# Performance work log

Hardware: AMD Instinct MI355X
Metric: run time of the kernel (lower is better)

## Reference

```python
import jax, jax.numpy as jnp
import numpy as np

N_STEPS = 2
MAX_STEP = 1.0
EPS64 = float(np.finfo(np.float64).eps)


def _sphere_log(p, q):
    # log map on unit sphere, tangent at p pointing to q; p,q: [..., D]
    cos = jnp.clip(jnp.sum(p * q, axis=-1, keepdims=True), -1.0, 1.0)
    u = q - cos * p
    un = jnp.linalg.norm(u, axis=-1, keepdims=True)
    theta = jnp.arccos(cos)
    return theta * u / (un + 1e-12)


def _sphere_exp(p, v):
    # exp map on unit sphere; jnp.sinc(n/pi) = sin(n)/n (stable at 0)
    n = jnp.linalg.norm(v, axis=-1, keepdims=True)
    x = jnp.cos(n) * p + jnp.sinc(n / jnp.pi) * v
    return x / jnp.linalg.norm(x, axis=-1, keepdims=True)


def setup_inputs() -> dict:
    key = jax.random.key(0)
    ks = jax.random.split(key, 6)
    N, C, D, E = 50000, 16, 3, 1600000
    nodes = jax.random.normal(ks[0], (N, C, D), dtype=jnp.float32)
    nodes = nodes / jnp.linalg.norm(nodes, axis=-1, keepdims=True)  # points on S^2
    edge_w = jax.random.uniform(ks[1], (E,), dtype=jnp.float32)
    senders = jax.random.randint(ks[2], (E,), 0, N, dtype=jnp.int32)
    receivers = jax.random.randint(ks[3], (E,), 0, N, dtype=jnp.int32)
    t_sqrt = 1.0 + 0.3 * jax.random.normal(ks[4], (C,), dtype=jnp.float32)
    delta_sqrt = 1.0 + 0.3 * jax.random.normal(ks[5], (C,), dtype=jnp.float32)
    return {"nodes": nodes, "edge_w": edge_w, "t_sqrt": t_sqrt,
            "delta_sqrt": delta_sqrt, "senders": senders, "receivers": receivers}


def reference(nodes, edge_w, t_sqrt, delta_sqrt, senders, receivers):
    N = nodes.shape[0]
    t = (t_sqrt ** 2) / N_STEPS            # per-channel time, split across Euler steps
    delta = delta_sqrt ** 2                 # per-channel min step size
    deg = jax.ops.segment_sum(edge_w, senders, num_segments=N)  # [N]

    def laplace(x):
        # graph Laplacian of manifold-valued signal: weighted mean of log maps, negated
        logs = _sphere_log(x[senders], x[receivers])              # [E, C, D]
        agg = jax.ops.segment_sum(edge_w[:, None, None] * logs, senders, num_segments=N)
        return -agg / (deg[:, None, None] + 1e-12)                # [N, C, D]

    def step(x, _):
        v = laplace(x)
        nrm = jnp.sqrt(jnp.sum(v * v, axis=-1) + EPS64)           # [N, C]
        alp = jax.nn.sigmoid(nrm - delta[None, :])
        scale = jnp.where(nrm * alp <= MAX_STEP, alp, MAX_STEP / nrm)
        v = -(v * scale[..., None]) * t[None, :, None]
        return _sphere_exp(x, v), None

    x, _ = jax.lax.scan(step, nodes, None, length=N_STEPS, unroll=N_STEPS)
    return x
```

## Files before the change

kernel.cpp:

```cpp
#include <hip/hip_runtime.h>
#include <math.h>


constexpr float EPS64F = 2.2204460492503131e-16f;
constexpr float PI_F   = 3.14159265358979323846f;
constexpr int   NREP   = 8;

typedef int   vi4 __attribute__((ext_vector_type(4)));
typedef float vf4 __attribute__((ext_vector_type(4)));

__global__ __launch_bounds__(256) void hist_kernel(
    const vi4* __restrict__ snd4, int* __restrict__ rep,
    vi4* __restrict__ pos4, const int* __restrict__ snd,
    int* __restrict__ pos, int N, int E) {
  int i = blockIdx.x * 256 + threadIdx.x;
  int rb = (blockIdx.x & (NREP - 1)) * N;
  int E4 = E >> 2;
  if (i < E4) {
    vi4 s = __builtin_nontemporal_load(&snd4[i]);
    vi4 p;
    p.x = atomicAdd(&rep[rb + s.x], 1);
    p.y = atomicAdd(&rep[rb + s.y], 1);
    p.z = atomicAdd(&rep[rb + s.z], 1);
    p.w = atomicAdd(&rep[rb + s.w], 1);
    __builtin_nontemporal_store(p, &pos4[i]);
  }
  if (i == 0) {
    for (int e = E4 << 2; e < E; ++e) pos[e] = atomicAdd(&rep[snd[e]], 1);
  }
}

__global__ __launch_bounds__(1024) void scanA_kernel(
    int* __restrict__ rep, int* __restrict__ row_start,
    int* __restrict__ btot, int N) {
  __shared__ int wsum[16];
  int tid = threadIdx.x;
  int lane = tid & 63, wave = tid >> 6;
  int i = blockIdx.x * 1024 + tid;
  int v = 0;
  if (i < N) {
    int run = 0;
    int cpre[NREP];
    #pragma unroll
    for (int r = 0; r < NREP; ++r) {
      int t = rep[r * N + i];
      cpre[r] = run;
      run += t;
    }
    v = run;
    #pragma unroll
    for (int r = 0; r < NREP; ++r) rep[r * N + i] = cpre[r];
  }
  int incl = v;
  #pragma unroll
  for (int off = 1; off < 64; off <<= 1) {
    int t = __shfl_up(incl, off, 64);
    if (lane >= off) incl += t;
  }
  if (lane == 63) wsum[wave] = incl;
  __syncthreads();
// ... 15 lines not shown
__global__ __launch_bounds__(64) void scanB_kernel(
    const int* __restrict__ btot, int* __restrict__ boff,
    int* __restrict__ row_start, int nb, int N) {
  int lane = threadIdx.x;
  int v = (lane < nb) ? btot[lane] : 0;
  int incl = v;
  #pragma unroll
  for (int off = 1; off < 64; off <<= 1) {
    int t = __shfl_up(incl, off, 64);
    if (lane >= off) incl += t;
  }
  if (lane < nb) boff[lane] = incl - v;
  if (lane == 63) row_start[N] = incl;
}

__global__ __launch_bounds__(1024) void scanC_kernel(
    int* __restrict__ row_start, const int* __restrict__ boff,
    int* __restrict__ rep, int N) {
  int i = blockIdx.x * 1024 + threadIdx.x;
  if (i < N) {
    int rs = row_start[i] + boff[blockIdx.x];
    row_start[i] = rs;
    #pragma unroll
    for (int r = 0; r < NREP; ++r) rep[r * N + i] += rs;
  }
}

__global__ __launch_bounds__(256) void fill_kernel(
    const vi4* __restrict__ snd4, const vi4* __restrict__ rcv4,
    const vf4* __restrict__ ew4, const vi4* __restrict__ pos4,
    const int* __restrict__ rep, long long* __restrict__ pair,
    const int* __restrict__ snd, const int* __restrict__ rcv,
    const float* __restrict__ ew, const int* __restrict__ pos, int N, int E) {
  int i = blockIdx.x * 256 + threadIdx.x;
  int rb = (blockIdx.x & (NREP - 1)) * N;
  int E4 = E >> 2;
  if (i < E4) {
    vi4 s = __builtin_nontemporal_load(&snd4[i]);
    vi4 r = __builtin_nontemporal_load(&rcv4[i]);
    vf4 w = __builtin_nontemporal_load(&ew4[i]);
    vi4 p = __builtin_nontemporal_load(&pos4[i]);
    pair[rep[rb + s.x] + p.x] =
        (long long)(((unsigned long long)(unsigned)__float_as_int(w.x) << 32) | (unsigned)r.x);
    pair[rep[rb + s.y] + p.y] =
        (long long)(((unsigned long long)(unsigned)__float_as_int(w.y) << 32) | (unsigned)r.y);
    pair[rep[rb + s.z] + p.z] =
        (long long)(((unsigned long long)(unsigned)__float_as_int(w.z) << 32) | (unsigned)r.z);
    pair[rep[rb + s.w] + p.w] =
        (long long)(((unsigned long long)(unsigned)__float_as_int(w.w) << 32) | (unsigned)r.w);
  }
  if (i == 0) {
    for (int e = E4 << 2; e < E; ++e) {
      pair[rep[snd[e]] + pos[e]] =
          (long long)(((unsigned long long)(unsigned)__float_as_int(ew[e]) << 32) | (unsigned)rcv[e]);
    }
  }
}

__device__ __forceinline__ void edge_accum(
    float p0, float p1, float p2, float q0, float q1, float q2, float w,
    float& a0, float& a1, float& a2) {
  float cs = fminf(1.0f, fmaxf(-1.0f, fmaf(p0, q0, fmaf(p1, q1, p2 * q2))));
  float u0 = fmaf(-cs, p0, q0);
  float u1 = fmaf(-cs, p1, q1);
  float u2 = fmaf(-cs, p2, q2);
  float un2 = fmaxf(fmaf(u0, u0, fmaf(u1, u1, u2 * u2)), 1e-24f);
  float ax = fabsf(cs);
  float s = sqrtf(1.0f - ax);
  float poly = fmaf(ax, fmaf(ax, fmaf(ax, -0.0187293f, 0.0742610f),
                             -0.2121144f), 1.5707288f);
  float th = s * poly;
  float theta = (cs >= 0.0f) ? th : (PI_F - th);
  float coef = w * theta * __builtin_amdgcn_rsqf(un2);
  a0 = fmaf(coef, u0, a0);
  a1 = fmaf(coef, u1, a1);
  a2 = fmaf(coef, u2, a2);
}

__global__ __launch_bounds__(256) void flow_kernel(
    const float* __restrict__ xin, const int* __restrict__ row_start,
    const long long* __restrict__ pair, const float* __restrict__ tsq,
    const float* __restrict__ dsq, float* __restrict__ xout, int N) {
  int node = blockIdx.x * 4 + (threadIdx.x >> 6);
  if (node >= N) return;
  int lane = threadIdx.x & 63;
  int c = lane & 15;
  int k = lane >> 4;
  int beg = row_start[node];
  int end = row_start[node + 1];
  int ip = node * 48 + c * 3;
  float p0 = xin[ip + 0], p1 = xin[ip + 1], p2 = xin[ip + 2];
  float a0 = 0.f, a1 = 0.f, a2 = 0.f, ws = 0.f;
  int iters = (end - beg + 7) >> 3;
  int lastj = end - 1;
  int j = beg + k;
  for (int t = 0; t < iters; ++t, j += 8) {
    int jA = j, jB = j + 4;
    long long eA = __builtin_nontemporal_load(&pair[min(jA, lastj)]);
    long long eB = __builtin_nontemporal_load(&pair[min(jB, lastj)]);
    int rA = (int)eA;
    int rB = (int)eB;
    float wA = (jA < end) ? __int_as_float((int)(eA >> 32)) : 0.f;
    float wB = (jB < end) ? __int_as_float((int)(eB >> 32)) : 0.f;
    const float* qA = xin + rA * 48 + c * 3;
    const float* qB = xin + rB * 48 + c * 3;
    float qA0 = qA[0], qA1 = qA[1], qA2 = qA[2];
    float qB0 = qB[0], qB1 = qB[1], qB2 = qB[2];
    edge_accum(p0, p1, p2, qA0, qA1, qA2, wA, a0, a1, a2);
    edge_accum(p0, p1, p2, qB0, qB1, qB2, wB, a0, a1, a2);
    ws += wA + wB;
  }
  a0 += __shfl_xor(a0, 16); a1 += __shfl_xor(a1, 16);
  a2 += __shfl_xor(a2, 16); ws += __shfl_xor(ws, 16);
  a0 += __shfl_xor(a0, 32); a1 += __shfl_xor(a1, 32);
  a2 += __shfl_xor(a2, 32); ws += __shfl_xor(ws, 32);
  float invdg = __builtin_amdgcn_rcpf(ws + 1e-12f);
  float g0 = a0 * invdg, g1 = a1 * invdg, g2 = a2 * invdg;
  float nrm = sqrtf(fmaf(g0, g0, fmaf(g1, g1, g2 * g2)) + EPS64F);
  float ts = tsq[c];
  float tch = ts * ts * 0.5f;
  float dsv = dsq[c];
  float dch = dsv * dsv;
  float alp = __builtin_amdgcn_rcpf(1.0f + __expf(dch - nrm));
  float scale = (nrm * alp <= 1.0f) ? alp : __builtin_amdgcn_rcpf(nrm);
  float f = scale * tch;
  float v0 = g0 * f, v1 = g1 * f, v2 = g2 * f;
  float nv = sqrtf(fmaf(v0, v0, fmaf(v1, v1, v2 * v2)));
  float cn = __cosf(nv);
  float sc = (nv > 1e-20f) ? (__sinf(nv) * __builtin_amdgcn_rcpf(nv)) : 1.0f;
  float y0 = fmaf(cn, p0, sc * v0);
  float y1 = fmaf(cn, p1, sc * v1);
  float y2 = fmaf(cn, p2, sc * v2);
  float inv = __builtin_amdgcn_rsqf(fmaf(y0, y0, fmaf(y1, y1, y2 * y2)));
  if (k == 0) {
    xout[ip + 0] = y0 * inv;
    xout[ip + 1] = y1 * inv;
    xout[ip + 2] = y2 * inv;
  }
}

extern "C" void kernel_launch(void* const* d_in, const int* in_sizes, int n_in,
                              void* d_out, int out_size, void* d_ws, size_t ws_size,
                              hipStream_t stream) {
  const float* nodes = (const float*)d_in[0];
  const float* ew    = (const float*)d_in[1];
  const float* tsq   = (const float*)d_in[2];
  const float* dsq   = (const float*)d_in[3];
  const int*   snd   = (const int*)d_in[4];
  const int*   rcv   = (const int*)d_in[5];
  float* out = (float*)d_out;

  int E = in_sizes[1];
  int N = in_sizes[0] / 48;

  int*       rep       = (int*)d_ws;
  int*       row_start = rep + NREP * N;
  int*       btot      = row_start + (N + 4);
  int*       boff      = btot + 64;
  long long* pair      = (long long*)(boff + 64);
  int*       pos       = (int*)(pair + E);
  float*     xtmp      = (float*)pos;

  hipMemsetAsync(rep, 0, sizeof(int) * (size_t)(NREP * N), stream);

  int E4 = E >> 2;
  int eb = (E4 + 255) / 256;
  int nb = (N + 1023) / 1024;
  int fb = (N + 3) / 4;

  hist_kernel<<<eb, 256, 0, stream>>>((const vi4*)snd, rep, (vi4*)pos,
                                      snd, pos, N, E);
  scanA_kernel<<<nb, 1024, 0, stream>>>(rep, row_start, btot, N);
  scanB_kernel<<<1, 64, 0, stream>>>(btot, boff, row_start, nb, N);
  scanC_kernel<<<nb, 1024, 0, stream>>>(row_start, boff, rep, N);
  fill_kernel<<<eb, 256, 0, stream>>>((const vi4*)snd, (const vi4*)rcv,
                                      (const vf4*)ew, (const vi4*)pos,
                                      rep, pair, snd, rcv, ew, pos, N, E);

  flow_kernel<<<fb, 256, 0, stream>>>(nodes, row_start, pair, tsq, dsq, xtmp, N);
  flow_kernel<<<fb, 256, 0, stream>>>(xtmp, row_start, pair, tsq, dsq, out, N);
}
```

Measured before the change: 300.0 us.

## Transpose node data to channel-major layout and stage CSR edges in LDS

```diff
diff --git a/kernel.cpp b/kernel.cpp
--- a/kernel.cpp
+++ b/kernel.cpp
@@ -5,27 +5,33 @@
 constexpr float EPS64F = 2.2204460492503131e-16f;
 constexpr float PI_F   = 3.14159265358979323846f;
 constexpr int   NREP   = 8;
+constexpr int   EDGE_CAP = 4096;
 
 typedef int   vi4 __attribute__((ext_vector_type(4)));
 typedef float vf4 __attribute__((ext_vector_type(4)));
+
 
 __global__ __launch_bounds__(256) void hist_kernel(
     const vi4* __restrict__ snd4, int* __restrict__ rep,
     vi4* __restrict__ pos4, const int* __restrict__ snd,
     int* __restrict__ pos, int N, int E) {
-  int i = blockIdx.x * 256 + threadIdx.x;
-  int rb = (blockIdx.x & (NREP - 1)) * N;
+  int tid = threadIdx.x;
   int E4 = E >> 2;
-  if (i < E4) {
-    vi4 s = __builtin_nontemporal_load(&snd4[i]);
-    vi4 p;
-    p.x = atomicAdd(&rep[rb + s.x], 1);
-    p.y = atomicAdd(&rep[rb + s.y], 1);
-    p.z = atomicAdd(&rep[rb + s.z], 1);
-    p.w = atomicAdd(&rep[rb + s.w], 1);
-    __builtin_nontemporal_store(p, &pos4[i]);
-  }
-  if (i == 0) {
+  #pragma unroll
+  for (int gg = 0; gg < 4; ++gg) {
+    int g = blockIdx.x * 1024 + gg * 256 + tid;
+    if (g < E4) {
+      int rb = (g & (NREP - 1)) * N;
+      vi4 s = __builtin_nontemporal_load(&snd4[g]);
+      vi4 p;
+      p.x = atomicAdd(&rep[rb + s.x], 1);
+      p.y = atomicAdd(&rep[rb + s.y], 1);
+      p.z = atomicAdd(&rep[rb + s.z], 1);
+      p.w = atomicAdd(&rep[rb + s.w], 1);
+      __builtin_nontemporal_store(p, &pos4[g]);
+    }
+  }
+  if (blockIdx.x == 0 && tid == 0) {
     for (int e = E4 << 2; e < E; ++e) pos[e] = atomicAdd(&rep[snd[e]], 1);
   }
 }
@@ -107,30 +113,82 @@
     const int* __restrict__ rep, long long* __restrict__ pair,
     const int* __restrict__ snd, const int* __restrict__ rcv,
     const float* __restrict__ ew, const int* __restrict__ pos, int N, int E) {
-  int i = blockIdx.x * 256 + threadIdx.x;
-  int rb = (blockIdx.x & (NREP - 1)) * N;
+  int tid = threadIdx.x;
   int E4 = E >> 2;
-  if (i < E4) {
-    vi4 s = __builtin_nontemporal_load(&snd4[i]);
-    vi4 r = __builtin_nontemporal_load(&rcv4[i]);
-    vf4 w = __builtin_nontemporal_load(&ew4[i]);
-    vi4 p = __builtin_nontemporal_load(&pos4[i]);
-    pair[rep[rb + s.x] + p.x] =
-        (long long)(((unsigned long long)(unsigned)__float_as_int(w.x) << 32) | (unsigned)r.x);
-    pair[rep[rb + s.y] + p.y] =
-        (long long)(((unsigned long long)(unsigned)__float_as_int(w.y) << 32) | (unsigned)r.y);
-    pair[rep[rb + s.z] + p.z] =
-        (long long)(((unsigned long long)(unsigned)__float_as_int(w.z) << 32) | (unsigned)r.z);
-    pair[rep[rb + s.w] + p.w] =
-        (long long)(((unsigned long long)(unsigned)__float_as_int(w.w) << 32) | (unsigned)r.w);
-  }
-  if (i == 0) {
+  #pragma unroll
+  for (int gg = 0; gg < 2; ++gg) {
+    int g = blockIdx.x * 512 + gg * 256 + tid;
+    if (g < E4) {
+      int rb = (g & (NREP - 1)) * N;
+      vi4 s = __builtin_nontemporal_load(&snd4[g]);
+      vi4 r = __builtin_nontemporal_load(&rcv4[g]);
+      vf4 w = __builtin_nontemporal_load(&ew4[g]);
+      vi4 p = __builtin_nontemporal_load(&pos4[g]);
+      pair[rep[rb + s.x] + p.x] =
+          (long long)(((unsigned long long)(unsigned)__float_as_int(w.x) << 32) | (unsigned)r.x);
+      pair[rep[rb + s.y] + p.y] =
+          (long long)(((unsigned long long)(unsigned)__float_as_int(w.y) << 32) | (unsigned)r.y);
+      pair[rep[rb + s.z] + p.z] =
+          (long long)(((unsigned long long)(unsigned)__float_as_int(w.z) << 32) | (unsigned)r.z);
+      pair[rep[rb + s.w] + p.w] =
+          (long long)(((unsigned long long)(unsigned)__float_as_int(w.w) << 32) | (unsigned)r.w);
+    }
+  }
+  if (blockIdx.x == 0 && tid == 0) {
     for (int e = E4 << 2; e < E; ++e) {
       pair[rep[snd[e]] + pos[e]] =
           (long long)(((unsigned long long)(unsigned)__float_as_int(ew[e]) << 32) | (unsigned)rcv[e]);
     }
   }
 }
+
+
+__global__ __launch_bounds__(256) void tfwd_kernel(
+    const float* __restrict__ x, float* __restrict__ xT, int N) {
+  __shared__ float tile[64 * 49];
+  int tid = threadIdx.x;
+  int b0 = blockIdx.x * 64;
+  int nmax = min(64, N - b0);
+  int total = nmax * 48;
+  const float* src = x + (size_t)b0 * 48;
+  for (int i = tid; i < total; i += 256) {
+    int nl = i / 48, jj = i - nl * 48;
+    tile[nl * 49 + jj] = src[i];
+  }
+  __syncthreads();
+  for (int i = tid; i < 3072; i += 256) {
+    int c = i / 192;
+    int rem = i - c * 192;
+    int nl = rem / 3;
+    int d = rem - nl * 3;
+    if (nl < nmax)
+      xT[(size_t)c * N * 3 + (size_t)(b0 + nl) * 3 + d] = tile[nl * 49 + c * 3 + d];
+  }
+}
+
+__global__ __launch_bounds__(256) void tbwd_kernel(
+    const float* __restrict__ xT, float* __restrict__ x, int N) {
+  __shared__ float tile[64 * 49];
+  int tid = threadIdx.x;
+  int b0 = blockIdx.x * 64;
+  int nmax = min(64, N - b0);
+  for (int i = tid; i < 3072; i += 256) {
+    int c = i / 192;
+    int rem = i - c * 192;
+    int nl = rem / 3;
+    int d = rem - nl * 3;
+    if (nl < nmax)
+      tile[nl * 49 + c * 3 + d] = xT[(size_t)c * N * 3 + (size_t)(b0 + nl) * 3 + d];
+  }
+  __syncthreads();
+  float* dst = x + (size_t)b0 * 48;
+  int total = nmax * 48;
+  for (int i = tid; i < total; i += 256) {
+    int nl = i / 48, jj = i - nl * 48;
+    dst[i] = tile[nl * 49 + jj];
+  }
+}
+
 
 __device__ __forceinline__ void edge_accum(
     float p0, float p1, float p2, float q0, float q1, float q2, float w,
@@ -152,7 +210,74 @@
   a2 = fmaf(coef, u2, a2);
 }
 
-__global__ __launch_bounds__(256) void flow_kernel(
+__device__ __forceinline__ void node_update(
+    float a0, float a1, float a2, float ws, float p0, float p1, float p2,
+    float ts, float dsv, float* dst) {
+  float invdg = __builtin_amdgcn_rcpf(ws + 1e-12f);
+  float g0 = a0 * invdg, g1 = a1 * invdg, g2 = a2 * invdg;
+  float nrm = sqrtf(fmaf(g0, g0, fmaf(g1, g1, g2 * g2)) + EPS64F);
+  float tch = ts * ts * 0.5f;
+  float dch = dsv * dsv;
+  float alp = __builtin_amdgcn_rcpf(1.0f + __expf(dch - nrm));
+  float scale = (nrm * alp <= 1.0f) ? alp : __builtin_amdgcn_rcpf(nrm);
+  float f = scale * tch;
+  float v0 = g0 * f, v1 = g1 * f, v2 = g2 * f;
+  float nv = sqrtf(fmaf(v0, v0, fmaf(v1, v1, v2 * v2)));
+  float cn = __cosf(nv);
+  float sc = (nv > 1e-20f) ? (__sinf(nv) * __builtin_amdgcn_rcpf(nv)) : 1.0f;
+  float y0 = fmaf(cn, p0, sc * v0);
+  float y1 = fmaf(cn, p1, sc * v1);
+  float y2 = fmaf(cn, p2, sc * v2);
+  float inv = __builtin_amdgcn_rsqf(fmaf(y0, y0, fmaf(y1, y1, y2 * y2)));
+  dst[0] = y0 * inv;
+  dst[1] = y1 * inv;
+  dst[2] = y2 * inv;
+}
+
+__global__ __launch_bounds__(256) void flowcm_kernel(
+    const float* __restrict__ xT, const int* __restrict__ row_start,
+    const long long* __restrict__ pair, const float* __restrict__ tsq,
+    const float* __restrict__ dsq, float* __restrict__ yT, int N) {
+  __shared__ long long spair[EDGE_CAP];
+  int tid = threadIdx.x;
+  int nloc = tid >> 2, k = tid & 3;
+  int b0 = blockIdx.x * 64;
+  int n = b0 + nloc;
+  int blkbeg = row_start[b0];
+  int blkend = row_start[min(b0 + 64, N)];
+  int staged = min(blkend - blkbeg, EDGE_CAP);
+  for (int i = tid; i < staged; i += 256) spair[i] = pair[blkbeg + i];
+  int beg = 0, end = 0;
+  if (n < N) { beg = row_start[n]; end = row_start[n + 1]; }
+  __syncthreads();
+  #pragma unroll 1
+  for (int c = 0; c < 16; ++c) {
+    const float* xc = xT + (size_t)c * N * 3;
+    float p0 = 0.f, p1 = 0.f, p2 = 0.f;
+    if (n < N) { p0 = xc[n * 3]; p1 = xc[n * 3 + 1]; p2 = xc[n * 3 + 2]; }
+    float a0 = 0.f, a1 = 0.f, a2 = 0.f, ws = 0.f;
+    for (int j = beg + k; j < end; j += 4) {
+      int idx = j - blkbeg;
+      long long e = (idx < staged) ? spair[idx]
+                                   : __builtin_nontemporal_load(&pair[j]);
+      int r = (int)e;
+      float w = __int_as_float((int)(e >> 32));
+      const float* q = xc + r * 3;
+      edge_accum(p0, p1, p2, q[0], q[1], q[2], w, a0, a1, a2);
+      ws += w;
+    }
+    a0 += __shfl_xor(a0, 1); a1 += __shfl_xor(a1, 1);
+    a2 += __shfl_xor(a2, 1); ws += __shfl_xor(ws, 1);
+    a0 += __shfl_xor(a0, 2); a1 += __shfl_xor(a1, 2);
+    a2 += __shfl_xor(a2, 2); ws += __shfl_xor(ws, 2);
+    if (k == 0 && n < N) {
+      node_update(a0, a1, a2, ws, p0, p1, p2, tsq[c], dsq[c],
+                  yT + (size_t)c * N * 3 + (size_t)n * 3);
+    }
+  }
+}
+
+__global__ __launch_bounds__(256) void flownc_kernel(
     const float* __restrict__ xin, const int* __restrict__ row_start,
     const long long* __restrict__ pair, const float* __restrict__ tsq,
     const float* __restrict__ dsq, float* __restrict__ xout, int N) {
@@ -189,29 +314,7 @@
   a2 += __shfl_xor(a2, 16); ws += __shfl_xor(ws, 16);
   a0 += __shfl_xor(a0, 32); a1 += __shfl_xor(a1, 32);
   a2 += __shfl_xor(a2, 32); ws += __shfl_xor(ws, 32);
-  float invdg = __builtin_amdgcn_rcpf(ws + 1e-12f);
-  float g0 = a0 * invdg, g1 = a1 * invdg, g2 = a2 * invdg;
-  float nrm = sqrtf(fmaf(g0, g0, fmaf(g1, g1, g2 * g2)) + EPS64F);
-  float ts = tsq[c];
-  float tch = ts * ts * 0.5f;
-  float dsv = dsq[c];
-  float dch = dsv * dsv;
-  float alp = __builtin_amdgcn_rcpf(1.0f + __expf(dch - nrm));
-  float scale = (nrm * alp <= 1.0f) ? alp : __builtin_amdgcn_rcpf(nrm);
-  float f = scale * tch;
-  float v0 = g0 * f, v1 = g1 * f, v2 = g2 * f;
-  float nv = sqrtf(fmaf(v0, v0, fmaf(v1, v1, v2 * v2)));
-  float cn = __cosf(nv);
-  float sc = (nv > 1e-20f) ? (__sinf(nv) * __builtin_amdgcn_rcpf(nv)) : 1.0f;
-  float y0 = fmaf(cn, p0, sc * v0);
-  float y1 = fmaf(cn, p1, sc * v1);
-  float y2 = fmaf(cn, p2, sc * v2);
-  float inv = __builtin_amdgcn_rsqf(fmaf(y0, y0, fmaf(y1, y1, y2 * y2)));
-  if (k == 0) {
-    xout[ip + 0] = y0 * inv;
-    xout[ip + 1] = y1 * inv;
-    xout[ip + 2] = y2 * inv;
-  }
+  if (k == 0) node_update(a0, a1, a2, ws, p0, p1, p2, tsq[c], dsq[c], xout + ip);
 }
 
 extern "C" void kernel_launch(void* const* d_in, const int* in_sizes, int n_in,
@@ -228,30 +331,51 @@
   int E = in_sizes[1];
   int N = in_sizes[0] / 48;
 
-  int*       rep       = (int*)d_ws;
-  int*       row_start = rep + NREP * N;
-  int*       btot      = row_start + (N + 4);
+  size_t repB  = (size_t)NREP * N * 4;
+  size_t rsB   = (size_t)(N + 4) * 4;
+  size_t auxB  = 128 * 4;
+  size_t pairB = (size_t)E * 8;
+  size_t xTB   = (size_t)N * 48 * 4;
+  size_t zzB   = xTB > (size_t)E * 4 ? xTB : (size_t)E * 4;
+  size_t need_cm = repB + rsB + auxB + pairB + xTB + zzB;
+
+  char* base = (char*)d_ws;
+  int*       rep       = (int*)base;
+  int*       row_start = (int*)(base + repB);
+  int*       btot      = (int*)(base + repB + rsB);
   int*       boff      = btot + 64;
-  long long* pair      = (long long*)(boff + 64);
-  int*       pos       = (int*)(pair + E);
-  float*     xtmp      = (float*)pos;
-
-  hipMemsetAsync(rep, 0, sizeof(int) * (size_t)(NREP * N), stream);
+  long long* pair      = (long long*)(base + repB + rsB + auxB);
+  float*     xT        = (float*)(base + repB + rsB + auxB + pairB);
+  float*     yT        = (float*)(base + repB + rsB + auxB + pairB + xTB);
+  bool cm = (ws_size >= need_cm);
+  int*   pos  = cm ? (int*)yT : (int*)xT;
+  float* xtmp = (float*)pos;
+
+  hipMemsetAsync(rep, 0, repB, stream);
 
   int E4 = E >> 2;
-  int eb = (E4 + 255) / 256;
+  int hb = (E4 + 1023) / 1024;
+  int fb = (E4 + 511) / 512;
   int nb = (N + 1023) / 1024;
-  int fb = (N + 3) / 4;
-
-  hist_kernel<<<eb, 256, 0, stream>>>((const vi4*)snd, rep, (vi4*)pos,
+  int tb = (N + 63) / 64;
+  int nfb = (N + 3) / 4;
+
+  if (cm) tfwd_kernel<<<tb, 256, 0, stream>>>(nodes, xT, N);
+  hist_kernel<<<hb, 256, 0, stream>>>((const vi4*)snd, rep, (vi4*)pos,
                                       snd, pos, N, E);
   scanA_kernel<<<nb, 1024, 0, stream>>>(rep, row_start, btot, N);
   scanB_kernel<<<1, 64, 0, stream>>>(btot, boff, row_start, nb, N);
   scanC_kernel<<<nb, 1024, 0, stream>>>(row_start, boff, rep, N);
-  fill_kernel<<<eb, 256, 0, stream>>>((const vi4*)snd, (const vi4*)rcv,
+  fill_kernel<<<fb, 256, 0, stream>>>((const vi4*)snd, (const vi4*)rcv,
                                       (const vf4*)ew, (const vi4*)pos,
                                       rep, pair, snd, rcv, ew, pos, N, E);
 
-  flow_kernel<<<fb, 256, 0, stream>>>(nodes, row_start, pair, tsq, dsq, xtmp, N);
-  flow_kernel<<<fb, 256, 0, stream>>>(xtmp, row_start, pair, tsq, dsq, out, N);
-}
+  if (cm) {
+    flowcm_kernel<<<tb, 256, 0, stream>>>(xT, row_start, pair, tsq, dsq, yT, N);
+    flowcm_kernel<<<tb, 256, 0, stream>>>(yT, row_start, pair, tsq, dsq, xT, N);
+    tbwd_kernel<<<tb, 256, 0, stream>>>(xT, out, N);
+  } else {
+    flownc_kernel<<<nfb, 256, 0, stream>>>(nodes, row_start, pair, tsq, dsq, xtmp, N);
+    flownc_kernel<<<nfb, 256, 0, stream>>>(xtmp, row_start, pair, tsq, dsq, out, N);
+  }
+}
```

New measurement: 473.1 us. +57.7%, slower.

## Gather neighbor points in padded fp16 with fp32 fallback for near-parallel pairs

Applied to the files above, without the earlier changes.

```diff
diff --git a/kernel.cpp b/kernel.cpp
--- a/kernel.cpp
+++ b/kernel.cpp
@@ -6,26 +6,32 @@
 constexpr float PI_F   = 3.14159265358979323846f;
 constexpr int   NREP   = 8;
 
-typedef int   vi4 __attribute__((ext_vector_type(4)));
-typedef float vf4 __attribute__((ext_vector_type(4)));
+typedef int      vi4 __attribute__((ext_vector_type(4)));
+typedef float    vf4 __attribute__((ext_vector_type(4)));
+typedef _Float16 vh4 __attribute__((ext_vector_type(4)));
+
 
 __global__ __launch_bounds__(256) void hist_kernel(
     const vi4* __restrict__ snd4, int* __restrict__ rep,
     vi4* __restrict__ pos4, const int* __restrict__ snd,
     int* __restrict__ pos, int N, int E) {
-  int i = blockIdx.x * 256 + threadIdx.x;
-  int rb = (blockIdx.x & (NREP - 1)) * N;
+  int tid = threadIdx.x;
   int E4 = E >> 2;
-  if (i < E4) {
-    vi4 s = __builtin_nontemporal_load(&snd4[i]);
-    vi4 p;
-    p.x = atomicAdd(&rep[rb + s.x], 1);
-    p.y = atomicAdd(&rep[rb + s.y], 1);
-    p.z = atomicAdd(&rep[rb + s.z], 1);
-    p.w = atomicAdd(&rep[rb + s.w], 1);
-    __builtin_nontemporal_store(p, &pos4[i]);
-  }
-  if (i == 0) {
+  #pragma unroll
+  for (int gg = 0; gg < 4; ++gg) {
+    int g = blockIdx.x * 1024 + gg * 256 + tid;
+    if (g < E4) {
+      int rb = (g & (NREP - 1)) * N;
+      vi4 s = __builtin_nontemporal_load(&snd4[g]);
+      vi4 p;
+      p.x = atomicAdd(&rep[rb + s.x], 1);
+      p.y = atomicAdd(&rep[rb + s.y], 1);
+      p.z = atomicAdd(&rep[rb + s.z], 1);
+      p.w = atomicAdd(&rep[rb + s.w], 1);
+      __builtin_nontemporal_store(p, &pos4[g]);
+    }
+  }
+  if (blockIdx.x == 0 && tid == 0) {
     for (int e = E4 << 2; e < E; ++e) pos[e] = atomicAdd(&rep[snd[e]], 1);
   }
 }
@@ -107,32 +113,49 @@
     const int* __restrict__ rep, long long* __restrict__ pair,
     const int* __restrict__ snd, const int* __restrict__ rcv,
     const float* __restrict__ ew, const int* __restrict__ pos, int N, int E) {
-  int i = blockIdx.x * 256 + threadIdx.x;
-  int rb = (blockIdx.x & (NREP - 1)) * N;
+  int tid = threadIdx.x;
   int E4 = E >> 2;
-  if (i < E4) {
-    vi4 s = __builtin_nontemporal_load(&snd4[i]);
-    vi4 r = __builtin_nontemporal_load(&rcv4[i]);
-    vf4 w = __builtin_nontemporal_load(&ew4[i]);
-    vi4 p = __builtin_nontemporal_load(&pos4[i]);
-    pair[rep[rb + s.x] + p.x] =
-        (long long)(((unsigned long long)(unsigned)__float_as_int(w.x) << 32) | (unsigned)r.x);
-    pair[rep[rb + s.y] + p.y] =
-        (long long)(((unsigned long long)(unsigned)__float_as_int(w.y) << 32) | (unsigned)r.y);
-    pair[rep[rb + s.z] + p.z] =
-        (long long)(((unsigned long long)(unsigned)__float_as_int(w.z) << 32) | (unsigned)r.z);
-    pair[rep[rb + s.w] + p.w] =
-        (long long)(((unsigned long long)(unsigned)__float_as_int(w.w) << 32) | (unsigned)r.w);
-  }
-  if (i == 0) {
+  #pragma unroll
+  for (int gg = 0; gg < 2; ++gg) {
+    int g = blockIdx.x * 512 + gg * 256 + tid;
+    if (g < E4) {
+      int rb = (g & (NREP - 1)) * N;
+      vi4 s = __builtin_nontemporal_load(&snd4[g]);
+      vi4 r = __builtin_nontemporal_load(&rcv4[g]);
+      vf4 w = __builtin_nontemporal_load(&ew4[g]);
+      vi4 p = __builtin_nontemporal_load(&pos4[g]);
+      pair[rep[rb + s.x] + p.x] =
+          (long long)(((unsigned long long)(unsigned)__float_as_int(w.x) << 32) | (unsigned)r.x);
+      pair[rep[rb + s.y] + p.y] =
+          (long long)(((unsigned long long)(unsigned)__float_as_int(w.y) << 32) | (unsigned)r.y);
+      pair[rep[rb + s.z] + p.z] =
+          (long long)(((unsigned long long)(unsigned)__float_as_int(w.z) << 32) | (unsigned)r.z);
+      pair[rep[rb + s.w] + p.w] =
+          (long long)(((unsigned long long)(unsigned)__float_as_int(w.w) << 32) | (unsigned)r.w);
+    }
+  }
+  if (blockIdx.x == 0 && tid == 0) {
     for (int e = E4 << 2; e < E; ++e) {
       pair[rep[snd[e]] + pos[e]] =
           (long long)(((unsigned long long)(unsigned)__float_as_int(ew[e]) << 32) | (unsigned)rcv[e]);
     }
-  }
-}
-
-__device__ __forceinline__ void edge_accum(
+    for (int z = 0; z < 16; ++z) pair[(size_t)E + z] = 0;
+  }
+}
+
+
+__global__ __launch_bounds__(256) void tconv_kernel(
+    const float* __restrict__ xf, _Float16* __restrict__ xh, int NC) {
+  int t = blockIdx.x * 256 + threadIdx.x;
+  if (t >= NC) return;
+  float a = xf[t * 3], b = xf[t * 3 + 1], d = xf[t * 3 + 2];
+  vh4 h;
+  h.x = (_Float16)a; h.y = (_Float16)b; h.z = (_Float16)d; h.w = (_Float16)0.f;
+  *(vh4*)(xh + (size_t)t * 4) = h;
+}
+
+
+__device__ __forceinline__ void edge_accum_f(
     float p0, float p1, float p2, float q0, float q1, float q2, float w,
     float& a0, float& a1, float& a2) {
   float cs = fminf(1.0f, fmaxf(-1.0f, fmaf(p0, q0, fmaf(p1, q1, p2 * q2))));
@@ -152,7 +175,112 @@
   a2 = fmaf(coef, u2, a2);
 }
 
-__global__ __launch_bounds__(256) void flow_kernel(
+__device__ __forceinline__ void edge_accum_h(
+    float p0, float p1, float p2, const _Float16* __restrict__ xh,
+    const float* __restrict__ xf, int r, int c, float w,
+    float& a0, float& a1, float& a2) {
+  vh4 qh = *(const vh4*)(xh + ((size_t)r * 16 + c) * 4);
+  float q0 = (float)qh.x, q1 = (float)qh.y, q2 = (float)qh.z;
+  float cs = fminf(1.0f, fmaxf(-1.0f, fmaf(p0, q0, fmaf(p1, q1, p2 * q2))));
+  float u0 = fmaf(-cs, p0, q0);
+  float u1 = fmaf(-cs, p1, q1);
+  float u2 = fmaf(-cs, p2, q2);
+  float un2 = fmaf(u0, u0, fmaf(u1, u1, u2 * u2));
+  if (un2 < 1e-4f && w > 0.f) {
+    const float* q = xf + (size_t)r * 48 + c * 3;
+    q0 = q[0]; q1 = q[1]; q2 = q[2];
+    cs = fminf(1.0f, fmaxf(-1.0f, fmaf(p0, q0, fmaf(p1, q1, p2 * q2))));
+    u0 = fmaf(-cs, p0, q0);
+    u1 = fmaf(-cs, p1, q1);
+    u2 = fmaf(-cs, p2, q2);
+    un2 = fmaf(u0, u0, fmaf(u1, u1, u2 * u2));
+  }
+  un2 = fmaxf(un2, 1e-24f);
+  float ax = fabsf(cs);
+  float s = sqrtf(1.0f - ax);
+  float poly = fmaf(ax, fmaf(ax, fmaf(ax, -0.0187293f, 0.0742610f),
+                             -0.2121144f), 1.5707288f);
+  float th = s * poly;
+  float theta = (cs >= 0.0f) ? th : (PI_F - th);
+  float coef = w * theta * __builtin_amdgcn_rsqf(un2);
+  a0 = fmaf(coef, u0, a0);
+  a1 = fmaf(coef, u1, a1);
+  a2 = fmaf(coef, u2, a2);
+}
+
+__device__ __forceinline__ void node_step(
+    float a0, float a1, float a2, float ws, float p0, float p1, float p2,
+    float ts, float dsv, float& y0, float& y1, float& y2) {
+  float invdg = __builtin_amdgcn_rcpf(ws + 1e-12f);
+  float g0 = a0 * invdg, g1 = a1 * invdg, g2 = a2 * invdg;
+  float nrm = sqrtf(fmaf(g0, g0, fmaf(g1, g1, g2 * g2)) + EPS64F);
+  float tch = ts * ts * 0.5f;
+  float dch = dsv * dsv;
+  float alp = __builtin_amdgcn_rcpf(1.0f + __expf(dch - nrm));
+  float scale = (nrm * alp <= 1.0f) ? alp : __builtin_amdgcn_rcpf(nrm);
+  float f = scale * tch;
+  float v0 = g0 * f, v1 = g1 * f, v2 = g2 * f;
+  float nv = sqrtf(fmaf(v0, v0, fmaf(v1, v1, v2 * v2)));
+  float cn = __cosf(nv);
+  float sc = (nv > 1e-20f) ? (__sinf(nv) * __builtin_amdgcn_rcpf(nv)) : 1.0f;
+  float t0 = fmaf(cn, p0, sc * v0);
+  float t1 = fmaf(cn, p1, sc * v1);
+  float t2 = fmaf(cn, p2, sc * v2);
+  float inv = __builtin_amdgcn_rsqf(fmaf(t0, t0, fmaf(t1, t1, t2 * t2)));
+  y0 = t0 * inv; y1 = t1 * inv; y2 = t2 * inv;
+}
+
+__global__ __launch_bounds__(256) void flowh_kernel(
+    const _Float16* __restrict__ xh, const float* __restrict__ xf,
+    const int* __restrict__ row_start, const long long* __restrict__ pair,
+    const float* __restrict__ tsq, const float* __restrict__ dsq,
+    float* __restrict__ yf, _Float16* __restrict__ yh, int N, int writeh) {
+  int node = blockIdx.x * 4 + (threadIdx.x >> 6);
+  if (node >= N) return;
+  int lane = threadIdx.x & 63;
+  int c = lane & 15;
+  int k = lane >> 4;
+  int beg = row_start[node];
+  int end = row_start[node + 1];
+  int ip = node * 48 + c * 3;
+  float p0 = xf[ip], p1 = xf[ip + 1], p2 = xf[ip + 2];
+  float a0 = 0.f, a1 = 0.f, a2 = 0.f, ws = 0.f;
+  int iters = (end - beg + 15) >> 4;
+  int j = beg + k;
+  for (int t = 0; t < iters; ++t, j += 16) {
+    long long e0 = __builtin_nontemporal_load(&pair[j]);
+    long long e1 = __builtin_nontemporal_load(&pair[j + 4]);
+    long long e2 = __builtin_nontemporal_load(&pair[j + 8]);
+    long long e3 = __builtin_nontemporal_load(&pair[j + 12]);
+    float w0 = (j      < end) ? __int_as_float((int)(e0 >> 32)) : 0.f;
+    float w1 = (j + 4  < end) ? __int_as_float((int)(e1 >> 32)) : 0.f;
+    float w2 = (j + 8  < end) ? __int_as_float((int)(e2 >> 32)) : 0.f;
+    float w3 = (j + 12 < end) ? __int_as_float((int)(e3 >> 32)) : 0.f;
+    int r0 = (int)e0, r1 = (int)e1, r2 = (int)e2, r3 = (int)e3;
+    edge_accum_h(p0, p1, p2, xh, xf, r0, c, w0, a0, a1, a2);
+    edge_accum_h(p0, p1, p2, xh, xf, r1, c, w1, a0, a1, a2);
+    edge_accum_h(p0, p1, p2, xh, xf, r2, c, w2, a0, a1, a2);
+    edge_accum_h(p0, p1, p2, xh, xf, r3, c, w3, a0, a1, a2);
+    ws += (w0 + w1) + (w2 + w3);
+  }
+  a0 += __shfl_xor(a0, 16); a1 += __shfl_xor(a1, 16);
+  a2 += __shfl_xor(a2, 16); ws += __shfl_xor(ws, 16);
+  a0 += __shfl_xor(a0, 32); a1 += __shfl_xor(a1, 32);
+  a2 += __shfl_xor(a2, 32); ws += __shfl_xor(ws, 32);
+  if (k == 0) {
+    float y0, y1, y2;
+    node_step(a0, a1, a2, ws, p0, p1, p2, tsq[c], dsq[c], y0, y1, y2);
+    yf[ip] = y0; yf[ip + 1] = y1; yf[ip + 2] = y2;
+    if (writeh) {
+      vh4 h;
+      h.x = (_Float16)y0; h.y = (_Float16)y1; h.z = (_Float16)y2;
+      h.w = (_Float16)0.f;
+      *(vh4*)(yh + ((size_t)node * 16 + c) * 4) = h;
+    }
+  }
+}
+
+__global__ __launch_bounds__(256) void flownc_kernel(
     const float* __restrict__ xin, const int* __restrict__ row_start,
     const long long* __restrict__ pair, const float* __restrict__ tsq,
     const float* __restrict__ dsq, float* __restrict__ xout, int N) {
@@ -164,55 +292,34 @@
   int beg = row_start[node];
   int end = row_start[node + 1];
   int ip = node * 48 + c * 3;
-  float p0 = xin[ip + 0], p1 = xin[ip + 1], p2 = xin[ip + 2];
+  float p0 = xin[ip], p1 = xin[ip + 1], p2 = xin[ip + 2];
   float a0 = 0.f, a1 = 0.f, a2 = 0.f, ws = 0.f;
   int iters = (end - beg + 7) >> 3;
-  int lastj = end - 1;
   int j = beg + k;
   for (int t = 0; t < iters; ++t, j += 8) {
-    int jA = j, jB = j + 4;
-    long long eA = __builtin_nontemporal_load(&pair[min(jA, lastj)]);
-    long long eB = __builtin_nontemporal_load(&pair[min(jB, lastj)]);
-    int rA = (int)eA;
-    int rB = (int)eB;
-    float wA = (jA < end) ? __int_as_float((int)(eA >> 32)) : 0.f;
-    float wB = (jB < end) ? __int_as_float((int)(eB >> 32)) : 0.f;
+    long long eA = __builtin_nontemporal_load(&pair[j]);
+    long long eB = __builtin_nontemporal_load(&pair[j + 4]);
+    int rA = (int)eA, rB = (int)eB;
+    float wA = (j     < end) ? __int_as_float((int)(eA >> 32)) : 0.f;
+    float wB = (j + 4 < end) ? __int_as_float((int)(eB >> 32)) : 0.f;
     const float* qA = xin + rA * 48 + c * 3;
     const float* qB = xin + rB * 48 + c * 3;
-    float qA0 = qA[0], qA1 = qA[1], qA2 = qA[2];
-    float qB0 = qB[0], qB1 = qB[1], qB2 = qB[2];
-    edge_accum(p0, p1, p2, qA0, qA1, qA2, wA, a0, a1, a2);
-    edge_accum(p0, p1, p2, qB0, qB1, qB2, wB, a0, a1, a2);
+    edge_accum_f(p0, p1, p2, qA[0], qA[1], qA[2], wA, a0, a1, a2);
+    edge_accum_f(p0, p1, p2, qB[0], qB[1], qB[2], wB, a0, a1, a2);
     ws += wA + wB;
   }
   a0 += __shfl_xor(a0, 16); a1 += __shfl_xor(a1, 16);
   a2 += __shfl_xor(a2, 16); ws += __shfl_xor(ws, 16);
   a0 += __shfl_xor(a0, 32); a1 += __shfl_xor(a1, 32);
   a2 += __shfl_xor(a2, 32); ws += __shfl_xor(ws, 32);
-  float invdg = __builtin_amdgcn_rcpf(ws + 1e-12f);
-  float g0 = a0 * invdg, g1 = a1 * invdg, g2 = a2 * invdg;
-  float nrm = sqrtf(fmaf(g0, g0, fmaf(g1, g1, g2 * g2)) + EPS64F);
-  float ts = tsq[c];
-  float tch = ts * ts * 0.5f;
-  float dsv = dsq[c];
-  float dch = dsv * dsv;
-  float alp = __builtin_amdgcn_rcpf(1.0f + __expf(dch - nrm));
-  float scale = (nrm * alp <= 1.0f) ? alp : __builtin_amdgcn_rcpf(nrm);
-  float f = scale * tch;
-  float v0 = g0 * f, v1 = g1 * f, v2 = g2 * f;
-  float nv = sqrtf(fmaf(v0, v0, fmaf(v1, v1, v2 * v2)));
-  float cn = __cosf(nv);
-  float sc = (nv > 1e-20f) ? (__sinf(nv) * __builtin_amdgcn_rcpf(nv)) : 1.0f;
-  float y0 = fmaf(cn, p0, sc * v0);
-  float y1 = fmaf(cn, p1, sc * v1);
-  float y2 = fmaf(cn, p2, sc * v2);
-  float inv = __builtin_amdgcn_rsqf(fmaf(y0, y0, fmaf(y1, y1, y2 * y2)));
   if (k == 0) {
-    xout[ip + 0] = y0 * inv;
-    xout[ip + 1] = y1 * inv;
-    xout[ip + 2] = y2 * inv;
-  }
-}
+    float y0, y1, y2;
+    node_step(a0, a1, a2, ws, p0, p1, p2, tsq[c], dsq[c], y0, y1, y2);
+    xout[ip] = y0; xout[ip + 1] = y1; xout[ip + 2] = y2;
+  }
+}
+
+static inline size_t al16(size_t x) { return (x + 15) & ~(size_t)15; }
 
 extern "C" void kernel_launch(void* const* d_in, const int* in_sizes, int n_in,
                               void* d_out, int out_size, void* d_ws, size_t ws_size,
@@ -228,30 +335,61 @@
   int E = in_sizes[1];
   int N = in_sizes[0] / 48;
 
-  int*       rep       = (int*)d_ws;
-  int*       row_start = rep + NREP * N;
-  int*       btot      = row_start + (N + 4);
+  size_t repB  = al16((size_t)NREP * N * 4);
+  size_t rsB   = al16((size_t)(N + 4) * 4);
+  size_t auxB  = 512;
+  size_t pairB = al16((size_t)(E + 16) * 8);
+  size_t xhB   = al16((size_t)N * 64 * 2);
+  size_t xf1B  = al16((size_t)N * 48 * 4);
+  size_t posB  = al16((size_t)E * 4);
+  size_t zB    = (posB > xhB) ? posB : xhB;
+  size_t need_h  = repB + rsB + auxB + pairB + xhB + xf1B + zB;
+  size_t z32B    = (posB > xf1B) ? posB : xf1B;
+  size_t need_32 = repB + rsB + auxB + pairB + z32B;
+
+  char* base = (char*)d_ws;
+  int*       rep       = (int*)base;
+  int*       row_start = (int*)(base + repB);
+  int*       btot      = (int*)(base + repB + rsB);
   int*       boff      = btot + 64;
-  long long* pair      = (long long*)(boff + 64);
-  int*       pos       = (int*)(pair + E);
-  float*     xtmp      = (float*)pos;
-
-  hipMemsetAsync(rep, 0, sizeof(int) * (size_t)(NREP * N), stream);
+  long long* pair      = (long long*)(base + repB + rsB + auxB);
+  char*      after     = base + repB + rsB + auxB + pairB;
+
+  bool hpath = (ws_size >= need_h);
+  _Float16* xh0  = (_Float16*)after;
+  float*    xf1  = (float*)(after + xhB);
+  char*     zreg = after + xhB + xf1B;
+  int*      pos  = hpath ? (int*)zreg : (int*)after;
+  _Float16* xh1  = (_Float16*)zreg;
+  float*    xtmp = (float*)after;
+
+  hipMemsetAsync(rep, 0, repB, stream);
 
   int E4 = E >> 2;
-  int eb = (E4 + 255) / 256;
-  int nb = (N + 1023) / 1024;
-  int fb = (N + 3) / 4;
-
-  hist_kernel<<<eb, 256, 0, stream>>>((const vi4*)snd, rep, (vi4*)pos,
+  int hb  = (E4 + 1023) / 1024;
+  int fbk = (E4 + 511) / 512;
+  int nb  = (N + 1023) / 1024;
+  int cb  = (N * 16 + 255) / 256;
+  int nfb = (N + 3) / 4;
+
+  if (hpath) tconv_kernel<<<cb, 256, 0, stream>>>(nodes, xh0, N * 16);
+  hist_kernel<<<hb, 256, 0, stream>>>((const vi4*)snd, rep, (vi4*)pos,
                                       snd, pos, N, E);
   scanA_kernel<<<nb, 1024, 0, stream>>>(rep, row_start, btot, N);
   scanB_kernel<<<1, 64, 0, stream>>>(btot, boff, row_start, nb, N);
   scanC_kernel<<<nb, 1024, 0, stream>>>(row_start, boff, rep, N);
-  fill_kernel<<<eb, 256, 0, stream>>>((const vi4*)snd, (const vi4*)rcv,
-                                      (const vf4*)ew, (const vi4*)pos,
-                                      rep, pair, snd, rcv, ew, pos, N, E);
-
-  flow_kernel<<<fb, 256, 0, stream>>>(nodes, row_start, pair, tsq, dsq, xtmp, N);
-  flow_kernel<<<fb, 256, 0, stream>>>(xtmp, row_start, pair, tsq, dsq, out, N);
-}
+  fill_kernel<<<fbk, 256, 0, stream>>>((const vi4*)snd, (const vi4*)rcv,
+                                       (const vf4*)ew, (const vi4*)pos,
+                                       rep, pair, snd, rcv, ew, pos, N, E);
+
+  if (hpath) {
+    flowh_kernel<<<nfb, 256, 0, stream>>>(xh0, nodes, row_start, pair,
+                                          tsq, dsq, xf1, xh1, N, 1);
+    flowh_kernel<<<nfb, 256, 0, stream>>>(xh1, xf1, row_start, pair,
+                                          tsq, dsq, out, (_Float16*)0, N, 0);
+  } else {
+    (void)need_32;
+    flownc_kernel<<<nfb, 256, 0, stream>>>(nodes, row_start, pair, tsq, dsq, xtmp, N);
+    flownc_kernel<<<nfb, 256, 0, stream>>>(xtmp, row_start, pair, tsq, dsq, out, N);
+  }
+}
```

Result: slower. 329.3 us (+9.8%).

## Pack edge math into float2, pre-scale receiver index, unroll edge loops

Applied to the files above, without the earlier changes.

```diff
diff --git a/kernel.cpp b/kernel.cpp
--- a/kernel.cpp
+++ b/kernel.cpp
@@ -8,24 +8,30 @@
 
 typedef int   vi4 __attribute__((ext_vector_type(4)));
 typedef float vf4 __attribute__((ext_vector_type(4)));
+typedef float vf2 __attribute__((ext_vector_type(2)));
+
 
 __global__ __launch_bounds__(256) void hist_kernel(
     const vi4* __restrict__ snd4, int* __restrict__ rep,
     vi4* __restrict__ pos4, const int* __restrict__ snd,
     int* __restrict__ pos, int N, int E) {
-  int i = blockIdx.x * 256 + threadIdx.x;
-  int rb = (blockIdx.x & (NREP - 1)) * N;
+  int tid = threadIdx.x;
   int E4 = E >> 2;
-  if (i < E4) {
-    vi4 s = __builtin_nontemporal_load(&snd4[i]);
-    vi4 p;
-    p.x = atomicAdd(&rep[rb + s.x], 1);
-    p.y = atomicAdd(&rep[rb + s.y], 1);
-    p.z = atomicAdd(&rep[rb + s.z], 1);
-    p.w = atomicAdd(&rep[rb + s.w], 1);
-    __builtin_nontemporal_store(p, &pos4[i]);
-  }
-  if (i == 0) {
+  #pragma unroll
+  for (int gg = 0; gg < 4; ++gg) {
+    int g = blockIdx.x * 1024 + gg * 256 + tid;
+    if (g < E4) {
+      int rb = (g & (NREP - 1)) * N;
+      vi4 s = __builtin_nontemporal_load(&snd4[g]);
+      vi4 p;
+      p.x = atomicAdd(&rep[rb + s.x], 1);
+      p.y = atomicAdd(&rep[rb + s.y], 1);
+      p.z = atomicAdd(&rep[rb + s.z], 1);
+      p.w = atomicAdd(&rep[rb + s.w], 1);
+      __builtin_nontemporal_store(p, &pos4[g]);
+    }
+  }
+  if (blockIdx.x == 0 && tid == 0) {
     for (int e = E4 << 2; e < E; ++e) pos[e] = atomicAdd(&rep[snd[e]], 1);
   }
 }
@@ -107,52 +113,88 @@
     const int* __restrict__ rep, long long* __restrict__ pair,
     const int* __restrict__ snd, const int* __restrict__ rcv,
     const float* __restrict__ ew, const int* __restrict__ pos, int N, int E) {
-  int i = blockIdx.x * 256 + threadIdx.x;
-  int rb = (blockIdx.x & (NREP - 1)) * N;
+  int tid = threadIdx.x;
   int E4 = E >> 2;
-  if (i < E4) {
-    vi4 s = __builtin_nontemporal_load(&snd4[i]);
-    vi4 r = __builtin_nontemporal_load(&rcv4[i]);
-    vf4 w = __builtin_nontemporal_load(&ew4[i]);
-    vi4 p = __builtin_nontemporal_load(&pos4[i]);
-    pair[rep[rb + s.x] + p.x] =
-        (long long)(((unsigned long long)(unsigned)__float_as_int(w.x) << 32) | (unsigned)r.x);
-    pair[rep[rb + s.y] + p.y] =
-        (long long)(((unsigned long long)(unsigned)__float_as_int(w.y) << 32) | (unsigned)r.y);
-    pair[rep[rb + s.z] + p.z] =
-        (long long)(((unsigned long long)(unsigned)__float_as_int(w.z) << 32) | (unsigned)r.z);
-    pair[rep[rb + s.w] + p.w] =
-        (long long)(((unsigned long long)(unsigned)__float_as_int(w.w) << 32) | (unsigned)r.w);
-  }
-  if (i == 0) {
+  #pragma unroll
+  for (int gg = 0; gg < 2; ++gg) {
+    int g = blockIdx.x * 512 + gg * 256 + tid;
+    if (g < E4) {
+      int rb = (g & (NREP - 1)) * N;
+      vi4 s = __builtin_nontemporal_load(&snd4[g]);
+      vi4 r = __builtin_nontemporal_load(&rcv4[g]);
+      vf4 w = __builtin_nontemporal_load(&ew4[g]);
+      vi4 p = __builtin_nontemporal_load(&pos4[g]);
+      pair[rep[rb + s.x] + p.x] =
+          (long long)(((unsigned long long)(unsigned)__float_as_int(w.x) << 32) | (unsigned)(r.x * 48));
+      pair[rep[rb + s.y] + p.y] =
+          (long long)(((unsigned long long)(unsigned)__float_as_int(w.y) << 32) | (unsigned)(r.y * 48));
+      pair[rep[rb + s.z] + p.z] =
+          (long long)(((unsigned long long)(unsigned)__float_as_int(w.z) << 32) | (unsigned)(r.z * 48));
+      pair[rep[rb + s.w] + p.w] =
+          (long long)(((unsigned long long)(unsigned)__float_as_int(w.w) << 32) | (unsigned)(r.w * 48));
+    }
+  }
+  if (blockIdx.x == 0 && tid == 0) {
     for (int e = E4 << 2; e < E; ++e) {
       pair[rep[snd[e]] + pos[e]] =
-          (long long)(((unsigned long long)(unsigned)__float_as_int(ew[e]) << 32) | (unsigned)rcv[e]);
-    }
-  }
-}
-
-__device__ __forceinline__ void edge_accum(
-    float p0, float p1, float p2, float q0, float q1, float q2, float w,
-    float& a0, float& a1, float& a2) {
-  float cs = fminf(1.0f, fmaxf(-1.0f, fmaf(p0, q0, fmaf(p1, q1, p2 * q2))));
-  float u0 = fmaf(-cs, p0, q0);
-  float u1 = fmaf(-cs, p1, q1);
-  float u2 = fmaf(-cs, p2, q2);
-  float un2 = fmaxf(fmaf(u0, u0, fmaf(u1, u1, u2 * u2)), 1e-24f);
-  float ax = fabsf(cs);
-  float s = sqrtf(1.0f - ax);
-  float poly = fmaf(ax, fmaf(ax, fmaf(ax, -0.0187293f, 0.0742610f),
-                             -0.2121144f), 1.5707288f);
-  float th = s * poly;
-  float theta = (cs >= 0.0f) ? th : (PI_F - th);
-  float coef = w * theta * __builtin_amdgcn_rsqf(un2);
-  a0 = fmaf(coef, u0, a0);
-  a1 = fmaf(coef, u1, a1);
-  a2 = fmaf(coef, u2, a2);
-}
-
-__global__ __launch_bounds__(256) void flow_kernel(
+          (long long)(((unsigned long long)(unsigned)__float_as_int(ew[e]) << 32) | (unsigned)(rcv[e] * 48));
+    }
+    for (int z = 0; z < 16; ++z) pair[(size_t)E + z] = 0;
+  }
+}
+
+
+__device__ __forceinline__ void edge_accum_pk(
+    vf2 p0, vf2 p1, vf2 p2, vf2 q0, vf2 q1, vf2 q2, vf2 w,
+    vf2& a0, vf2& a1, vf2& a2) {
+  vf2 cs = p0 * q0 + p1 * q1 + p2 * q2;
+  cs = __builtin_elementwise_min(vf2{1.f, 1.f},
+       __builtin_elementwise_max(vf2{-1.f, -1.f}, cs));
+  vf2 u0 = q0 - cs * p0;
+  vf2 u1 = q1 - cs * p1;
+  vf2 u2 = q2 - cs * p2;
+  vf2 un2 = __builtin_elementwise_max(u0 * u0 + u1 * u1 + u2 * u2,
+                                      vf2{1e-24f, 1e-24f});
+  vf2 ax = __builtin_elementwise_abs(cs);
+  vf2 s = __builtin_elementwise_sqrt(vf2{1.f, 1.f} - ax);
+  vf2 poly = ((ax * -0.0187293f + 0.0742610f) * ax - 0.2121144f) * ax
+             + 1.5707288f;
+  vf2 th = s * poly;
+  vf2 theta;
+  theta.x = (cs.x >= 0.0f) ? th.x : (PI_F - th.x);
+  theta.y = (cs.y >= 0.0f) ? th.y : (PI_F - th.y);
+  vf2 rsq;
+  rsq.x = __builtin_amdgcn_rsqf(un2.x);
+  rsq.y = __builtin_amdgcn_rsqf(un2.y);
+  vf2 coef = w * theta * rsq;
+  a0 += coef * u0;
+  a1 += coef * u1;
+  a2 += coef * u2;
+}
+
+__device__ __forceinline__ void node_step(
+    float a0, float a1, float a2, float ws, float p0, float p1, float p2,
+    float ts, float dsv, float& y0, float& y1, float& y2) {
+  float invdg = __builtin_amdgcn_rcpf(ws + 1e-12f);
+  float g0 = a0 * invdg, g1 = a1 * invdg, g2 = a2 * invdg;
+  float nrm = sqrtf(fmaf(g0, g0, fmaf(g1, g1, g2 * g2)) + EPS64F);
+  float tch = ts * ts * 0.5f;
+  float dch = dsv * dsv;
+  float alp = __builtin_amdgcn_rcpf(1.0f + __expf(dch - nrm));
+  float scale = (nrm * alp <= 1.0f) ? alp : __builtin_amdgcn_rcpf(nrm);
+  float f = scale * tch;
+  float v0 = g0 * f, v1 = g1 * f, v2 = g2 * f;
+  float nv = sqrtf(fmaf(v0, v0, fmaf(v1, v1, v2 * v2)));
+  float cn = __cosf(nv);
+  float sc = (nv > 1e-20f) ? (__sinf(nv) * __builtin_amdgcn_rcpf(nv)) : 1.0f;
+  float t0 = fmaf(cn, p0, sc * v0);
+  float t1 = fmaf(cn, p1, sc * v1);
+  float t2 = fmaf(cn, p2, sc * v2);
+  float inv = __builtin_amdgcn_rsqf(fmaf(t0, t0, fmaf(t1, t1, t2 * t2)));
+  y0 = t0 * inv; y1 = t1 * inv; y2 = t2 * inv;
+}
+
+__global__ __launch_bounds__(256) void flowp_kernel(
     const float* __restrict__ xin, const int* __restrict__ row_start,
     const long long* __restrict__ pair, const float* __restrict__ tsq,
     const float* __restrict__ dsq, float* __restrict__ xout, int N) {
@@ -161,58 +203,53 @@
   int lane = threadIdx.x & 63;
   int c = lane & 15;
   int k = lane >> 4;
+  int c3 = c * 3;
   int beg = row_start[node];
   int end = row_start[node + 1];
-  int ip = node * 48 + c * 3;
-  float p0 = xin[ip + 0], p1 = xin[ip + 1], p2 = xin[ip + 2];
-  float a0 = 0.f, a1 = 0.f, a2 = 0.f, ws = 0.f;
-  int iters = (end - beg + 7) >> 3;
-  int lastj = end - 1;
+  int ip = node * 48 + c3;
+  float ps0 = xin[ip], ps1 = xin[ip + 1], ps2 = xin[ip + 2];
+  vf2 p0 = {ps0, ps0}, p1 = {ps1, ps1}, p2 = {ps2, ps2};
+  vf2 a0 = {0.f, 0.f}, a1 = {0.f, 0.f}, a2 = {0.f, 0.f}, wsv = {0.f, 0.f};
+  int iters = (end - beg + 15) >> 4;
   int j = beg + k;
-  for (int t = 0; t < iters; ++t, j += 8) {
-    int jA = j, jB = j + 4;
-    long long eA = __builtin_nontemporal_load(&pair[min(jA, lastj)]);
-    long long eB = __builtin_nontemporal_load(&pair[min(jB, lastj)]);
-    int rA = (int)eA;
-    int rB = (int)eB;
-    float wA = (jA < end) ? __int_as_float((int)(eA >> 32)) : 0.f;
-    float wB = (jB < end) ? __int_as_float((int)(eB >> 32)) : 0.f;
-    const float* qA = xin + rA * 48 + c * 3;
-    const float* qB = xin + rB * 48 + c * 3;
-    float qA0 = qA[0], qA1 = qA[1], qA2 = qA[2];
-    float qB0 = qB[0], qB1 = qB[1], qB2 = qB[2];
-    edge_accum(p0, p1, p2, qA0, qA1, qA2, wA, a0, a1, a2);
-    edge_accum(p0, p1, p2, qB0, qB1, qB2, wB, a0, a1, a2);
-    ws += wA + wB;
-  }
-  a0 += __shfl_xor(a0, 16); a1 += __shfl_xor(a1, 16);
-  a2 += __shfl_xor(a2, 16); ws += __shfl_xor(ws, 16);
-  a0 += __shfl_xor(a0, 32); a1 += __shfl_xor(a1, 32);
-  a2 += __shfl_xor(a2, 32); ws += __shfl_xor(ws, 32);
-  float invdg = __builtin_amdgcn_rcpf(ws + 1e-12f);
-  float g0 = a0 * invdg, g1 = a1 * invdg, g2 = a2 * invdg;
-  float nrm = sqrtf(fmaf(g0, g0, fmaf(g1, g1, g2 * g2)) + EPS64F);
-  float ts = tsq[c];
-  float tch = ts * ts * 0.5f;
-  float dsv = dsq[c];
-  float dch = dsv * dsv;
-  float alp = __builtin_amdgcn_rcpf(1.0f + __expf(dch - nrm));
-  float scale = (nrm * alp <= 1.0f) ? alp : __builtin_amdgcn_rcpf(nrm);
-  float f = scale * tch;
-  float v0 = g0 * f, v1 = g1 * f, v2 = g2 * f;
-  float nv = sqrtf(fmaf(v0, v0, fmaf(v1, v1, v2 * v2)));
-  float cn = __cosf(nv);
-  float sc = (nv > 1e-20f) ? (__sinf(nv) * __builtin_amdgcn_rcpf(nv)) : 1.0f;
-  float y0 = fmaf(cn, p0, sc * v0);
-  float y1 = fmaf(cn, p1, sc * v1);
-  float y2 = fmaf(cn, p2, sc * v2);
-  float inv = __builtin_amdgcn_rsqf(fmaf(y0, y0, fmaf(y1, y1, y2 * y2)));
+  for (int t = 0; t < iters; ++t, j += 16) {
+    long long e0 = __builtin_nontemporal_load(&pair[j]);
+    long long e1 = __builtin_nontemporal_load(&pair[j + 4]);
+    long long e2 = __builtin_nontemporal_load(&pair[j + 8]);
+    long long e3 = __builtin_nontemporal_load(&pair[j + 12]);
+    float w0 = (j      < end) ? __int_as_float((int)(e0 >> 32)) : 0.f;
+    float w1 = (j + 4  < end) ? __int_as_float((int)(e1 >> 32)) : 0.f;
+    float w2 = (j + 8  < end) ? __int_as_float((int)(e2 >> 32)) : 0.f;
+    float w3 = (j + 12 < end) ? __int_as_float((int)(e3 >> 32)) : 0.f;
+    const float* q0p = xin + ((int)e0 + c3);
+    const float* q1p = xin + ((int)e1 + c3);
+    const float* q2p = xin + ((int)e2 + c3);
+    const float* q3p = xin + ((int)e3 + c3);
+    float qa0 = q0p[0], qa1 = q0p[1], qa2 = q0p[2];
+    float qb0 = q1p[0], qb1 = q1p[1], qb2 = q1p[2];
+    float qc0 = q2p[0], qc1 = q2p[1], qc2 = q2p[2];
+    float qd0 = q3p[0], qd1 = q3p[1], qd2 = q3p[2];
+    vf2 wA = {w0, w1}, wB = {w2, w3};
+    edge_accum_pk(p0, p1, p2, vf2{qa0, qb0}, vf2{qa1, qb1}, vf2{qa2, qb2},
+                  wA, a0, a1, a2);
+    edge_accum_pk(p0, p1, p2, vf2{qc0, qd0}, vf2{qc1, qd1}, vf2{qc2, qd2},
+                  wB, a0, a1, a2);
+    wsv += wA + wB;
+  }
+  float A0 = a0.x + a0.y, A1 = a1.x + a1.y, A2 = a2.x + a2.y;
+  float ws = wsv.x + wsv.y;
+  A0 += __shfl_xor(A0, 16); A1 += __shfl_xor(A1, 16);
+  A2 += __shfl_xor(A2, 16); ws += __shfl_xor(ws, 16);
+  A0 += __shfl_xor(A0, 32); A1 += __shfl_xor(A1, 32);
+  A2 += __shfl_xor(A2, 32); ws += __shfl_xor(ws, 32);
   if (k == 0) {
-    xout[ip + 0] = y0 * inv;
-    xout[ip + 1] = y1 * inv;
-    xout[ip + 2] = y2 * inv;
-  }
-}
+    float y0, y1, y2;
+    node_step(A0, A1, A2, ws, ps0, ps1, ps2, tsq[c], dsq[c], y0, y1, y2);
+    xout[ip] = y0; xout[ip + 1] = y1; xout[ip + 2] = y2;
+  }
+}
+
+static inline size_t al16(size_t x) { return (x + 15) & ~(size_t)15; }
 
 extern "C" void kernel_launch(void* const* d_in, const int* in_sizes, int n_in,
                               void* d_out, int out_size, void* d_ws, size_t ws_size,
@@ -228,30 +265,38 @@
   int E = in_sizes[1];
   int N = in_sizes[0] / 48;
 
-  int*       rep       = (int*)d_ws;
-  int*       row_start = rep + NREP * N;
-  int*       btot      = row_start + (N + 4);
+  size_t repB  = al16((size_t)NREP * N * 4);
+  size_t rsB   = al16((size_t)(N + 4) * 4);
+  size_t auxB  = 512;
+  size_t pairB = al16((size_t)(E + 16) * 8);
+
+  char* base = (char*)d_ws;
+  int*       rep       = (int*)base;
+  int*       row_start = (int*)(base + repB);
+  int*       btot      = (int*)(base + repB + rsB);
   int*       boff      = btot + 64;
-  long long* pair      = (long long*)(boff + 64);
-  int*       pos       = (int*)(pair + E);
-  float*     xtmp      = (float*)pos;
-
-  hipMemsetAsync(rep, 0, sizeof(int) * (size_t)(NREP * N), stream);
+  long long* pair      = (long long*)(base + repB + rsB + auxB);
+  char*      after     = base + repB + rsB + auxB + pairB;
+  int*       pos       = (int*)after;
+  float*     xtmp      = (float*)after;
+
+  hipMemsetAsync(rep, 0, repB, stream);
 
   int E4 = E >> 2;
-  int eb = (E4 + 255) / 256;
-  int nb = (N + 1023) / 1024;
-  int fb = (N + 3) / 4;
-
-  hist_kernel<<<eb, 256, 0, stream>>>((const vi4*)snd, rep, (vi4*)pos,
+  int hb  = (E4 + 1023) / 1024;
+  int fbk = (E4 + 511) / 512;
+  int nb  = (N + 1023) / 1024;
+  int nfb = (N + 3) / 4;
+
+  hist_kernel<<<hb, 256, 0, stream>>>((const vi4*)snd, rep, (vi4*)pos,
                                       snd, pos, N, E);
   scanA_kernel<<<nb, 1024, 0, stream>>>(rep, row_start, btot, N);
   scanB_kernel<<<1, 64, 0, stream>>>(btot, boff, row_start, nb, N);
   scanC_kernel<<<nb, 1024, 0, stream>>>(row_start, boff, rep, N);
-  fill_kernel<<<eb, 256, 0, stream>>>((const vi4*)snd, (const vi4*)rcv,
-                                      (const vf4*)ew, (const vi4*)pos,
-                                      rep, pair, snd, rcv, ew, pos, N, E);
-
-  flow_kernel<<<fb, 256, 0, stream>>>(nodes, row_start, pair, tsq, dsq, xtmp, N);
-  flow_kernel<<<fb, 256, 0, stream>>>(xtmp, row_start, pair, tsq, dsq, out, N);
-}
+  fill_kernel<<<fbk, 256, 0, stream>>>((const vi4*)snd, (const vi4*)rcv,
+                                       (const vf4*)ew, (const vi4*)pos,
+                                       rep, pair, snd, rcv, ew, pos, N, E);
+
+  flowp_kernel<<<nfb, 256, 0, stream>>>(nodes, row_start, pair, tsq, dsq, xtmp, N);
+  flowp_kernel<<<nfb, 256, 0, stream>>>(xtmp, row_start, pair, tsq, dsq, out, N);
+}
```

Measured after the change: 309.1 us. 3.0% more time.
